# Performance work log

Measured on AMD Instinct MI355X. Metric: run time of the kernel, lower is better.

## Reference

```python
import jax, jax.numpy as jnp
import numpy as np

N_PLANT = 16  # width of x_p inside xi; y = x_p since output_fn is None


def _solve_implicit(x_k, y, Cv, Dvw, Dvy):
    """Solve v = Cv x_k + Dvw phi(v) + Dvy y for w = phi(v) by backward sweep.

    Dvw is strictly upper triangular, so sweeping rows i = n_w-1 .. 0 gives
    the exact solution. Carry W is [n_w, B]; rows not yet solved are zero,
    so Dvw[i] @ W only picks up already-solved columns j > i (exactly the
    torch loop's math).
    """
    base = x_k @ Cv.T + y @ Dvy.T          # [B, n_w]
    baseT = base.T                          # [n_w, B]
    n_w = Dvw.shape[0]

    def step(W, i):
        v_i = baseT[i] + Dvw[i] @ W         # [B]
        W = W.at[i].set(jax.nn.relu(v_i))
        return W, None

    W0 = jnp.zeros_like(baseT)
    W, _ = jax.lax.scan(step, W0, jnp.arange(n_w - 1, -1, -1))
    return W.T                              # [B, n_w]


def setup_inputs() -> dict:
    key = jax.random.key(0)
    ks = jax.random.split(key, 7)
    B, n_k, n_w, n_y, n_u = 131072, 64, 128, N_PLANT, 16
    xi = jax.random.normal(ks[0], (B, N_PLANT + n_k), dtype=jnp.float32)
    Cv = jax.random.normal(ks[1], (n_w, n_k), dtype=jnp.float32) / np.float32(np.sqrt(n_k))
    # strictly upper triangular, scaled for stability of the ReLU sweep
    Dvw = jnp.triu(jax.random.normal(ks[2], (n_w, n_w), dtype=jnp.float32), 1) / np.float32(np.sqrt(n_w))
    Dvy = jax.random.normal(ks[3], (n_w, n_y), dtype=jnp.float32) / np.float32(np.sqrt(n_y))
    Cu = jax.random.normal(ks[4], (n_u, n_k), dtype=jnp.float32) / np.float32(np.sqrt(n_k))
    Duw = jax.random.normal(ks[5], (n_u, n_w), dtype=jnp.float32) / np.float32(np.sqrt(n_w))
    Duy = jax.random.normal(ks[6], (n_u, n_y), dtype=jnp.float32) / np.float32(np.sqrt(n_y))
    return {"xi": xi, "Cv": Cv, "Dvw": Dvw, "Dvy": Dvy, "Cu": Cu, "Duw": Duw, "Duy": Duy}


def reference(xi, Cv, Dvw, Dvy, Cu, Duw, Duy):
    x_p = xi[:, :N_PLANT]
    x_k = xi[:, N_PLANT:]
    y = x_p  # output_fn is None
    w = _solve_implicit(x_k, y, Cv, Dvw, Dvy)
    u = x_k @ Cu.T + w @ Duw.T + y @ Duy.T  # [B, n_u]
    return u
```

## Files before the change

### kernel.cpp

```cpp
#include <hip/hip_runtime.h>


#define NW 128
#define NK 64
#define NY 16
#define NU 16
#define NXI 80

#define DENSE_OFF 0
#define SOLVE_OFF 23040
#define DIAG_OFF  41472
#define BLOB_BYTES 49664
#define N_PREP_THREADS 12416

typedef _Float16 f16;
typedef __attribute__((ext_vector_type(4))) _Float16 f16x4;
typedef __attribute__((ext_vector_type(8))) _Float16 f16x8;
typedef __attribute__((ext_vector_type(4))) float f32x4;

template<int I> struct Ic { static constexpr int value = I; };
template<int I, int N, typename F>
__device__ __forceinline__ void ufor(F&& f) {
    if constexpr (I < N) { f(Ic<I>{}); ufor<I + 1, N>(static_cast<F&&>(f)); }
}

__device__ __forceinline__ float emat_val(int i, int k,
                                          const float* Cv, const float* Dvy,
                                          const float* Cu, const float* Duy) {
    if (i < NW) return (k < NY) ? Dvy[i * NY + k] : Cv[i * NK + (k - NY)];
    int r = i - NW;
    return (k < NY) ? Duy[r * NY + k] : Cu[r * NK + (k - NY)];
}

__global__ void prep(const float* __restrict__ Cv, const float* __restrict__ Dvw,
                     const float* __restrict__ Dvy, const float* __restrict__ Cu,
                     const float* __restrict__ Duw, const float* __restrict__ Duy,
                     unsigned int* __restrict__ ws) {
    int id = blockIdx.x * 256 + threadIdx.x;
    if (id >= N_PREP_THREADS) return;
    if (id < DIAG_OFF / 4) {
        int byte = id * 4;
        float v0, v1;
        if (byte < SOLVE_OFF) {
            int T = byte / 2560, rem = byte % 2560;
            int l, i0, kbase;
            if (rem < 2048) {
                int chunk = rem >> 10, cb = rem & 1023;
                l = cb >> 4; i0 = (cb & 15) >> 1;
                kbase = chunk * 32 + (l >> 4) * 8;
            } else {
                int cb = rem - 2048;
                l = cb >> 3; i0 = (cb & 7) >> 1;
                kbase = 64 + (l >> 4) * 4;
            }
            int row = T * 16 + (l & 15);
            v0 = emat_val(row, kbase + i0,     Cv, Dvy, Cu, Duy);
            v1 = emat_val(row, kbase + i0 + 1, Cv, Dvy, Cu, Duy);
        } else {
            int sb = byte - SOLVE_OFF;
            int f = sb >> 9, cb = sb & 511;
            int l = cb >> 3, i0 = (cb & 7) >> 1;
            int kk = (l >> 4) * 4 + i0;
            if (f < 28) {
                int K = 1; while ((K + 1) * K / 2 <= f) K++;
                int J = f - K * (K - 1) / 2;
                int row = J * 16 + (l & 15);
                v0 = Dvw[row * NW + K * 16 + kk];
                v1 = Dvw[row * NW + K * 16 + kk + 1];
            } else {
                int K = f - 28;
                int r = l & 15;
                v0 = Duw[r * NW + K * 16 + kk];
                v1 = Duw[r * NW + K * 16 + kk + 1];
            }
        }
        union { _Float16 h[2]; unsigned u; } p;
        p.h[0] = (_Float16)v0; p.h[1] = (_Float16)v1;
        ws[id] = p.u;
    } else {
        int d = id - DIAG_OFF / 4;
        int blk = d >> 8, rem = d & 255, j = rem >> 4, ii = rem & 15;
        ((float*)ws)[id] = Dvw[(blk * 16 + ii) * NW + blk * 16 + j];
    }
}

__global__ __launch_bounds__(512, 4) void rinn_mfma(const float* __restrict__ xi,
                                                    const unsigned char* __restrict__ wsb,
                                                    float* __restrict__ out) {
    __shared__ __align__(16) unsigned char LDS[BLOB_BYTES];
    const int tid = threadIdx.x;
    const int lane = tid & 63;
    const int wv = tid >> 6;
    const int g = lane >> 4;
    const int c = lane & 15;
    const int batch0 = (blockIdx.x * 8 + wv) * 16;
    const float* __restrict__ xb = xi + (size_t)(batch0 + c) * NXI;

    const float4 xA0 = *(const float4*)(xb + 0 * 32 + g * 8);
    const float4 xA1 = *(const float4*)(xb + 0 * 32 + g * 8 + 4);
    const float4 xB0 = *(const float4*)(xb + 1 * 32 + g * 8);
    const float4 xB1 = *(const float4*)(xb + 1 * 32 + g * 8 + 4);
    const float4 xC  = *(const float4*)(xb + 64 + g * 4);

    {
        const uint4* src = (const uint4*)wsb;
        uint4* dst = (uint4*)LDS;
        ufor<0, 6>([&](auto IT) { dst[IT.value * 512 + tid] = src[IT.value * 512 + tid]; });
        if (tid < 32) dst[3072 + tid] = src[3072 + tid];
    }
    __syncthreads();

    f32x4 acc[9];
    ufor<0, 9>([&](auto T) { acc[T.value] = (f32x4){0.f, 0.f, 0.f, 0.f}; });

    ufor<0, 2>([&](auto KC) {
        constexpr int kc = KC.value;
        const float4 xa = (kc == 0) ? xA0 : xB0;
        const float4 xc2 = (kc == 0) ? xA1 : xB1;
        f16x8 Bf;
        Bf[0] = (f16)xa.x; Bf[1] = (f16)xa.y; Bf[2] = (f16)xa.z; Bf[3] = (f16)xa.w;
        Bf[4] = (f16)xc2.x; Bf[5] = (f16)xc2.y; Bf[6] = (f16)xc2.z; Bf[7] = (f16)xc2.w;
        ufor<0, 9>([&](auto T) {
            constexpr int t = T.value;
            const f16x8 Af = *(const f16x8*)&LDS[t * 2560 + kc * 1024 + lane * 16];
            acc[t] = __builtin_amdgcn_mfma_f32_16x16x32_f16(Af, Bf, acc[t], 0, 0, 0);
        });
    });
    {
        f16x4 Bf;
        Bf[0] = (f16)xC.x; Bf[1] = (f16)xC.y; Bf[2] = (f16)xC.z; Bf[3] = (f16)xC.w;
        ufor<0, 9>([&](auto T) {
            constexpr int t = T.value;
            const f16x4 Af = *(const f16x4*)&LDS[t * 2560 + 2048 + lane * 8];
            acc[t] = __builtin_amdgcn_mfma_f32_16x16x16f16(Af, Bf, acc[t], 0, 0, 0);
        });
    }

    const unsigned char* __restrict__ diagp = &LDS[DIAG_OFF + g * 16];

    ufor<0, 8>([&](auto QQ) {
        constexpr int K = 7 - QQ.value;
        ufor<0, 16>([&](auto JJ) {
            constexpr int j = 15 - JJ.value;
            constexpr int gj = j >> 2, rj = j & 3;
            float s = __shfl(acc[K][rj], gj * 16 + c, 64);
            float w = fmaxf(s, 0.f);
            const f32x4 d = *(const f32x4*)(diagp + (K * 16 + j) * 64);
            acc[K][0] = fmaf(d[0], w, acc[K][0]);
            acc[K][1] = fmaf(d[1], w, acc[K][1]);
            acc[K][2] = fmaf(d[2], w, acc[K][2]);
            acc[K][3] = fmaf(d[3], w, acc[K][3]);
        });
        f16x4 Wf;
        Wf[0] = (f16)fmaxf(acc[K][0], 0.f);
        Wf[1] = (f16)fmaxf(acc[K][1], 0.f);
        Wf[2] = (f16)fmaxf(acc[K][2], 0.f);
        Wf[3] = (f16)fmaxf(acc[K][3], 0.f);
        {
            const f16x4 Af = *(const f16x4*)&LDS[SOLVE_OFF + (28 + K) * 512 + lane * 8];
            acc[8] = __builtin_amdgcn_mfma_f32_16x16x16f16(Af, Wf, acc[8], 0, 0, 0);
        }
        ufor<0, K>([&](auto JB) {
            constexpr int J = JB.value;
            const f16x4 Af = *(const f16x4*)&LDS[SOLVE_OFF + (K * (K - 1) / 2 + J) * 512 + lane * 8];
            acc[J] = __builtin_amdgcn_mfma_f32_16x16x16f16(Af, Wf, acc[J], 0, 0, 0);
        });
    });

    float4 o = make_float4(acc[8][0], acc[8][1], acc[8][2], acc[8][3]);
    *(float4*)(out + (size_t)(batch0 + c) * NU + g * 4) = o;
}

extern "C" void kernel_launch(void* const* d_in, const int* in_sizes, int n_in,
                              void* d_out, int out_size, void* d_ws, size_t ws_size,
                              hipStream_t stream) {
    const float* xi  = (const float*)d_in[0];
    const float* Cv  = (const float*)d_in[1];
    const float* Dvw = (const float*)d_in[2];
    const float* Dvy = (const float*)d_in[3];
    const float* Cu  = (const float*)d_in[4];
    const float* Duw = (const float*)d_in[5];
    const float* Duy = (const float*)d_in[6];
    float* out = (float*)d_out;

    const int B = in_sizes[0] / NXI;

    prep<<<(N_PREP_THREADS + 255) / 256, 256, 0, stream>>>(
        Cv, Dvw, Dvy, Cu, Duw, Duy, (unsigned int*)d_ws);
    rinn_mfma<<<B / 128, 512, 0, stream>>>(
        xi, (const unsigned char*)d_ws, out);
}
```

Measured before the change: 111.9 us.

## Solve diagonal triangular blocks redundantly per lane after one upfront shuffle gather

For each 16x16 diagonal block of the backward sweep, all 16 pre-activation values are now gathered with independent shuffles up front. Each lane then runs the full triangular solve in registers, reading the diagonal coefficients directly from global memory with wave-uniform addresses. This removes the serial chain of dependent shuffle, LDS-load and FMA steps and drops the diagonal blob from shared memory, which shrinks the LDS footprint. In exchange every lane does about 120 FMAs of redundant work per block and needs more registers. The off-diagonal MFMA updates are also issued in reverse order.

```diff
diff --git a/kernel.cpp b/kernel.cpp
--- a/kernel.cpp
+++ b/kernel.cpp
@@ -10,6 +10,7 @@
 #define DENSE_OFF 0
 #define SOLVE_OFF 23040
 #define DIAG_OFF  41472
+#define LDS_BYTES 41472
 #define BLOB_BYTES 49664
 #define N_PREP_THREADS 12416
 
@@ -87,7 +88,7 @@
 __global__ __launch_bounds__(512, 4) void rinn_mfma(const float* __restrict__ xi,
                                                     const unsigned char* __restrict__ wsb,
                                                     float* __restrict__ out) {
-    __shared__ __align__(16) unsigned char LDS[BLOB_BYTES];
+    __shared__ __align__(16) unsigned char LDS[LDS_BYTES];
     const int tid = threadIdx.x;
     const int lane = tid & 63;
     const int wv = tid >> 6;
@@ -95,6 +96,7 @@
     const int c = lane & 15;
     const int batch0 = (blockIdx.x * 8 + wv) * 16;
     const float* __restrict__ xb = xi + (size_t)(batch0 + c) * NXI;
+    const float* __restrict__ diag = (const float*)(wsb + DIAG_OFF);
 
     const float4 xA0 = *(const float4*)(xb + 0 * 32 + g * 8);
     const float4 xA1 = *(const float4*)(xb + 0 * 32 + g * 8 + 4);
@@ -105,8 +107,8 @@
     {
         const uint4* src = (const uint4*)wsb;
         uint4* dst = (uint4*)LDS;
-        ufor<0, 6>([&](auto IT) { dst[IT.value * 512 + tid] = src[IT.value * 512 + tid]; });
-        if (tid < 32) dst[3072 + tid] = src[3072 + tid];
+        ufor<0, 5>([&](auto IT) { dst[IT.value * 512 + tid] = src[IT.value * 512 + tid]; });
+        if (tid < 32) dst[2560 + tid] = src[2560 + tid];
     }
     __syncthreads();
 
@@ -136,32 +138,40 @@
         });
     }
 
-    const unsigned char* __restrict__ diagp = &LDS[DIAG_OFF + g * 16];
-
     ufor<0, 8>([&](auto QQ) {
         constexpr int K = 7 - QQ.value;
+
+        float s[16];
+        ufor<0, 16>([&](auto JJ) {
+            constexpr int j = JJ.value;
+            s[j] = __shfl(acc[K][j & 3], (j >> 2) * 16 + c, 64);
+        });
+
+        float w[16];
         ufor<0, 16>([&](auto JJ) {
             constexpr int j = 15 - JJ.value;
-            constexpr int gj = j >> 2, rj = j & 3;
-            float s = __shfl(acc[K][rj], gj * 16 + c, 64);
-            float w = fmaxf(s, 0.f);
-            const f32x4 d = *(const f32x4*)(diagp + (K * 16 + j) * 64);
-            acc[K][0] = fmaf(d[0], w, acc[K][0]);
-            acc[K][1] = fmaf(d[1], w, acc[K][1]);
-            acc[K][2] = fmaf(d[2], w, acc[K][2]);
-            acc[K][3] = fmaf(d[3], w, acc[K][3]);
-        });
+            const float wj = fmaxf(s[j], 0.f);
+            w[j] = wj;
+            ufor<0, j>([&](auto II) {
+                constexpr int i = II.value;
+                s[i] = fmaf(diag[(K * 16 + j) * 16 + i], wj, s[i]);
+            });
+        });
+
         f16x4 Wf;
-        Wf[0] = (f16)fmaxf(acc[K][0], 0.f);
-        Wf[1] = (f16)fmaxf(acc[K][1], 0.f);
-        Wf[2] = (f16)fmaxf(acc[K][2], 0.f);
-        Wf[3] = (f16)fmaxf(acc[K][3], 0.f);
+        ufor<0, 4>([&](auto RR) {
+            constexpr int r = RR.value;
+            const float wr = (g == 0) ? w[r] : (g == 1) ? w[4 + r]
+                           : (g == 2) ? w[8 + r] : w[12 + r];
+            Wf[r] = (f16)wr;
+        });
+
         {
             const f16x4 Af = *(const f16x4*)&LDS[SOLVE_OFF + (28 + K) * 512 + lane * 8];
             acc[8] = __builtin_amdgcn_mfma_f32_16x16x16f16(Af, Wf, acc[8], 0, 0, 0);
         }
         ufor<0, K>([&](auto JB) {
-            constexpr int J = JB.value;
+            constexpr int J = K - 1 - JB.value;
             const f16x4 Af = *(const f16x4*)&LDS[SOLVE_OFF + (K * (K - 1) / 2 + J) * 512 + lane * 8];
             acc[J] = __builtin_amdgcn_mfma_f32_16x16x16f16(Af, Wf, acc[J], 0, 0, 0);
         });
```

Result: slower. 121.8 us (+8.9%).
